# Kernel tuning notes

Hardware: AMD Instinct MI355X
Metric: run time of the kernel (lower is better)

The kernel has to match this reference:

```python
import jax, jax.numpy as jnp
import numpy as np

NEG_INF = jnp.float32(-1e30)  # stand-in for -inf; relu(-inf) == relu(-1e30) == 0


def setup_inputs() -> dict:
    key = jax.random.key(0)
    ks = jax.random.split(key, 8)
    B, S, E = 4, 4096, 512
    query = jax.random.normal(ks[0], (B, S, E), dtype=jnp.float32)
    k_in = jax.random.normal(ks[1], (B, S, E), dtype=jnp.float32)
    v_in = jax.random.normal(ks[2], (B, S, E), dtype=jnp.float32)
    mask = jax.random.randint(ks[3], (B, S, S), 0, 2) > 0  # bool [B,S,S]
    scale = 1.0 / np.sqrt(E)
    W1 = jax.random.uniform(ks[4], (E, E), jnp.float32, -scale, scale)
    b1 = jax.random.uniform(ks[5], (E,), jnp.float32, -scale, scale)
    W2 = jax.random.uniform(ks[6], (E, E), jnp.float32, -scale, scale)
    b2 = jax.random.uniform(ks[7], (E,), jnp.float32, -scale, scale)
    return {"query": query, "key": k_in, "value": v_in, "mask": mask,
            "W1": W1, "b1": b1, "W2": W2, "b2": b2}


def reference(query, key, value, mask, W1, b1, W2, b2):
    # key projection: nn.Linear -> x @ W.T + b
    k = jnp.einsum('bse,fe->bsf', key, W1) + b1
    # raw dot-product correlation scores [B, S, S]
    scores = jnp.einsum('bqe,bke->bqk', query, k)
    # module forces mask[:, :, 0] = True, then fills ~mask with -inf
    m = mask.at[:, :, 0].set(True)
    scores = jnp.where(m, scores, NEG_INF)
    # ReLU instead of softmax (no normalization); dropout is identity in eval
    alpha = jax.nn.relu(scores)
    # value projection then AV matmul
    v = jnp.einsum('bse,fe->bsf', value, W2) + b2
    out = jnp.einsum('bqk,bke->bqe', alpha, v)
    return out
```

## Files before the change

### kernel.cpp

```cpp
#include <hip/hip_runtime.h>
#include <cstdint>


typedef __bf16 bf16x8 __attribute__((ext_vector_type(8)));
typedef float f32x4 __attribute__((ext_vector_type(4)));

__device__ __forceinline__ unsigned short f2bf(float f) {
  unsigned int u = __float_as_uint(f);
  u += 0x7fffu + ((u >> 16) & 1u);
  return (unsigned short)(u >> 16);
}

__device__ __forceinline__ void async_load16(const void* g, void* l) {
  __builtin_amdgcn_global_load_lds(
      (const __attribute__((address_space(1))) unsigned int*)(uintptr_t)g,
      (__attribute__((address_space(3))) unsigned int*)(unsigned int)(uintptr_t)l,
      16, 0, 0);
}

__global__ void __launch_bounds__(256)
prep(const float* __restrict__ q, const float* __restrict__ k,
     const float* __restrict__ v, const float* __restrict__ w1,
     const float* __restrict__ w2, const int* __restrict__ m,
     unsigned short* __restrict__ qb, unsigned short* __restrict__ kb,
     unsigned short* __restrict__ vb, unsigned short* __restrict__ w1b,
     unsigned short* __restrict__ w2b, unsigned int* __restrict__ bits) {
  const int b = blockIdx.x, tid = threadIdx.x;
  if (b < 24576) {
    const int which = b >> 13;
    const int idx = (b & 8191) * 256 + tid;
    const float* in = (which == 0) ? q : (which == 1) ? k : v;
    unsigned short* out = (which == 0) ? qb : (which == 1) ? kb : vb;
    float4 f = ((const float4*)in)[idx];
    ushort4 o;
    o.x = f2bf(f.x); o.y = f2bf(f.y); o.z = f2bf(f.z); o.w = f2bf(f.w);
    ((ushort4*)out)[idx] = o;
  } else if (b < 25088) {
    const int which = (b - 24576) >> 8;
    const int idx = ((b - 24576) & 255) * 256 + tid;
    const float* in = (which == 0) ? w1 : w2;
    unsigned short* out = (which == 0) ? w1b : w2b;
    float4 f = ((const float4*)in)[idx];
    ushort4 o;
    o.x = f2bf(f.x); o.y = f2bf(f.y); o.z = f2bf(f.z); o.w = f2bf(f.w);
    ((ushort4*)out)[idx] = o;
  } else {
    const int lane = tid & 63;
    const size_t wid = (size_t)(b - 25088) * 4 + (tid >> 6);
    const size_t base = wid * 256;
    unsigned long long bl[4];
#pragma unroll
    for (int c = 0; c < 4; ++c) {
      size_t e = base + (size_t)c * 64 + lane;
      int col = (int)(e & 4095);
      bl[c] = __ballot((m[e] != 0) || (col == 0));
    }
    if (lane < 8)
      bits[base / 32 + lane] = (unsigned int)(bl[lane >> 1] >> ((lane & 1) * 32));
  }
}

__global__ void __launch_bounds__(256)
proj(const unsigned short* __restrict__ Kb, const unsigned short* __restrict__ W1b,
     unsigned short* __restrict__ Kp, const float* __restrict__ b1,
     const unsigned short* __restrict__ W2b, const unsigned short* __restrict__ Vb,
     unsigned short* __restrict__ Vpt, const float* __restrict__ b2) {
  constexpr int K = 512;
  constexpr long long SE = 4096LL * 512;
  __shared__ unsigned short sA[2 * 128 * 32];
  __shared__ unsigned short sB[2 * 128 * 32];

  const int L = blockIdx.x;
  const unsigned short *Ab, *Bb;
  unsigned short* C;
  const float* bias;
  int tm0, tn0, N, epi;
  if (L < 512) {
    tn0 = (L & 3) * 128; tm0 = (L >> 2) * 128;
    Ab = Kb; Bb = W1b; C = Kp; bias = b1; N = 512; epi = 0;
  } else {
    const int t = L - 512;
    tn0 = (t & 31) * 128; tm0 = ((t >> 5) & 3) * 128;
    const int bz = t >> 7;
    Ab = W2b; Bb = Vb + (size_t)bz * SE; C = Vpt + (size_t)bz * SE;
    bias = b2; N = 4096; epi = 1;
  }

  const int tid = threadIdx.x;
  const int lane = tid & 63, wave = tid >> 6;
  const int ldrow = lane >> 2, lcol = (lane & 3) * 8;
  const int wm = (wave >> 1) * 64, wn = (wave & 1) * 64;
  const int lr = lane & 15, lq = lane >> 4;

  f32x4 acc[4][4] = {};

  for (int k0 = 0; k0 < K; k0 += 64) {
#pragma unroll
    for (int g = 0; g < 2; ++g)
#pragma unroll
      for (int l = 0; l < 2; ++l) {
        const int row = wave * 32 + l * 16;
        async_load16(Ab + (size_t)(tm0 + row + ldrow) * K + (k0 + g * 32 + lcol),
                     &sA[g * 4096 + row * 32]);
        async_load16(Bb + (size_t)(tn0 + row + ldrow) * K + (k0 + g * 32 + lcol),
                     &sB[g * 4096 + row * 32]);
      }
    __syncthreads();
#pragma unroll
    for (int g = 0; g < 2; ++g) {
      bf16x8 af[4], bfr[4];
#pragma unroll
      for (int t = 0; t < 4; ++t) {
        af[t]  = *(const bf16x8*)&sA[g * 4096 + (wm + t * 16 + lr) * 32 + lq * 8];
        bfr[t] = *(const bf16x8*)&sB[g * 4096 + (wn + t * 16 + lr) * 32 + lq * 8];
      }
#pragma unroll
      for (int mt = 0; mt < 4; ++mt)
#pragma unroll
        for (int nt = 0; nt < 4; ++nt)
          acc[mt][nt] = __builtin_amdgcn_mfma_f32_16x16x32_bf16(af[mt], bfr[nt],
                                                                acc[mt][nt], 0, 0, 0);
    }
    __syncthreads();
  }

#pragma unroll
  for (int mt = 0; mt < 4; ++mt)
#pragma unroll
    for (int r = 0; r < 4; ++r) {
      const int mm = tm0 + wm + mt * 16 + lq * 4 + r;
#pragma unroll
      for (int nt = 0; nt < 4; ++nt) {
        const int n = tn0 + wn + nt * 16 + lr;
        float v = acc[mt][nt][r];
        v += (epi == 0) ? bias[n] : bias[mm];
        C[(size_t)mm * N + n] = f2bf(v);
      }
    }
}

template <int EPI>
__global__ void __launch_bounds__(512, 2)
gemm256(const unsigned short* __restrict__ A, const unsigned short* __restrict__ B,
        void* __restrict__ Cout, const unsigned int* __restrict__ mbits,
        int M, int N, int K,
        long long strA, long long strB, long long strC, long long strM) {
  __shared__ unsigned short sA[2][256][64];
  __shared__ unsigned short sB[2][256][64];

  int lin = blockIdx.x;
  lin = (lin & 7) * ((int)gridDim.x >> 3) + (lin >> 3);
  const int tilesN = N >> 8;
  const int tilesM = M >> 8;
  const int bx = lin % tilesN;
  const int by = (lin / tilesN) % tilesM;
  const int bz = lin / (tilesN * tilesM);

  const int tn0 = bx << 8, tm0 = by << 8;
  const unsigned short* Ab = A + (size_t)bz * strA;
  const unsigned short* Bb = B + (size_t)bz * strB;

  const int tid  = threadIdx.x;
  const int lane = tid & 63;
  const int w    = tid >> 6;
  const int wr   = w >> 2;
  const int wc   = w & 3;
  const int lr   = lane & 15;
  const int lq   = lane >> 4;

  const int srow = tid >> 3;
  const int scol = (((tid & 7) ^ (srow & 7)) << 3);
  const int sdst = tid << 4;

#define STAGE64(bufbase, g, t0, k0, R0)                                      \
  async_load16((g) + (size_t)((t0) + (R0) + srow) * K + (k0) + scol,         \
               (char*)(bufbase) + ((R0) << 7) + sdst)

  const int sxor  = (lr & 7) << 4;
  const int k0off = (lq << 4) ^ sxor;
  const int k1off = (64 | (lq << 4)) ^ sxor;
  const int aRow  = (wr * 128 + lr) * 128;
  const int bRow  = (wc * 64 + lr) * 128;

#define LDA(d, mh, mt2, kk)                                                  \
  (*(const bf16x8*)((const char*)sA[d] + aRow + (mh) * 8192 + (mt2) * 2048 + \
                    k##kk##off))
#define LDB(d, nh, nt2, kk)                                                  \
  (*(const bf16x8*)((const char*)sB[d] + bRow + (nh) * 4096 + (nt2) * 2048 + \
                    k##kk##off))

  f32x4 acc[8][4] = {};
  bf16x8 afr[4][2];
  bf16x8 bfr[4][2];

#define RDA(d, mh)                                                           \
  _Pragma("unroll") for (int mt2 = 0; mt2 < 4; ++mt2) {                      \
    afr[mt2][0] = LDA(d, mh, mt2, 0);                                        \
    afr[mt2][1] = LDA(d, mh, mt2, 1);                                        \
  }
#define RDB(d, nh)                                                           \
  _Pragma("unroll") for (int nt2 = 0; nt2 < 2; ++nt2) {                      \
    bfr[(nh) * 2 + nt2][0] = LDB(d, nh, nt2, 0);                             \
    bfr[(nh) * 2 + nt2][1] = LDB(d, nh, nt2, 1);                             \
  }
#define MFMAQ(mh, nh)                                                        \
  __builtin_amdgcn_s_setprio(1);                                             \
  _Pragma("unroll") for (int mt2 = 0; mt2 < 4; ++mt2)                        \
  _Pragma("unroll") for (int nt2 = 0; nt2 < 2; ++nt2) {                      \
    acc[(mh) * 4 + mt2][(nh) * 2 + nt2] =                                    \
        __builtin_amdgcn_mfma_f32_16x16x32_bf16(                             \
            afr[mt2][0], bfr[(nh) * 2 + nt2][0],                             \
            acc[(mh) * 4 + mt2][(nh) * 2 + nt2], 0, 0, 0);                   \
    acc[(mh) * 4 + mt2][(nh) * 2 + nt2] =                                    \
        __builtin_amdgcn_mfma_f32_16x16x32_bf16(                             \
            afr[mt2][1], bfr[(nh) * 2 + nt2][1],                             \
            acc[(mh) * 4 + mt2][(nh) * 2 + nt2], 0, 0, 0);                   \
  }                                                                          \
  __builtin_amdgcn_s_setprio(0);
#define BAR __builtin_amdgcn_s_barrier()

  const int nIter = K >> 7;

  STAGE64(sB[0], Bb, tn0, 0, 0);   STAGE64(sB[0], Bb, tn0, 0, 64);
  STAGE64(sB[0], Bb, tn0, 0, 128); STAGE64(sB[0], Bb, tn0, 0, 192);
  STAGE64(sA[0], Ab, tm0, 0, 0);   STAGE64(sA[0], Ab, tm0, 0, 64);
  STAGE64(sA[0], Ab, tm0, 0, 128); STAGE64(sA[0], Ab, tm0, 0, 192);
  STAGE64(sB[1], Bb, tn0, 64, 0);  STAGE64(sB[1], Bb, tn0, 64, 64);
  STAGE64(sB[1], Bb, tn0, 64, 128);STAGE64(sB[1], Bb, tn0, 64, 192);
  asm volatile("s_waitcnt vmcnt(4)" ::: "memory");
  BAR;

  for (int j = 0; j < nIter; ++j) {
    const int kb = j << 7;
    const bool pf = (j + 1 < nIter);
    RDA(0, 0); RDB(0, 0);
    STAGE64(sA[1], Ab, tm0, kb + 64, 0);
    STAGE64(sA[1], Ab, tm0, kb + 64, 64);
    BAR; MFMAQ(0, 0); BAR;
    RDB(0, 1);
    STAGE64(sA[1], Ab, tm0, kb + 64, 128);
    STAGE64(sA[1], Ab, tm0, kb + 64, 192);
    BAR; MFMAQ(0, 1); BAR;
    RDA(0, 1);
    if (pf) { STAGE64(sB[0], Bb, tn0, kb + 128, 0);
              STAGE64(sB[0], Bb, tn0, kb + 128, 64); }
    BAR; MFMAQ(1, 1); BAR;
    if (pf) { STAGE64(sB[0], Bb, tn0, kb + 128, 128);
              STAGE64(sB[0], Bb, tn0, kb + 128, 192); }
    BAR; MFMAQ(1, 0);
    if (pf) asm volatile("s_waitcnt vmcnt(4)" ::: "memory");
    else    asm volatile("s_waitcnt vmcnt(0)" ::: "memory");
    BAR;
    RDA(1, 0); RDB(1, 0);
    if (pf) { STAGE64(sA[0], Ab, tm0, kb + 128, 0);
              STAGE64(sA[0], Ab, tm0, kb + 128, 64); }
    BAR; MFMAQ(0, 0); BAR;
    RDB(1, 1);
    if (pf) { STAGE64(sA[0], Ab, tm0, kb + 128, 128);
              STAGE64(sA[0], Ab, tm0, kb + 128, 192); }
    BAR; MFMAQ(0, 1); BAR;
    RDA(1, 1);
    if (pf) { STAGE64(sB[1], Bb, tn0, kb + 192, 0);
              STAGE64(sB[1], Bb, tn0, kb + 192, 64); }
    BAR; MFMAQ(1, 1); BAR;
    if (pf) { STAGE64(sB[1], Bb, tn0, kb + 192, 128);
              STAGE64(sB[1], Bb, tn0, kb + 192, 192); }
    BAR; MFMAQ(1, 0);
    asm volatile("s_waitcnt vmcnt(4)" ::: "memory");
    BAR;
  }

#pragma unroll
  for (int mt = 0; mt < 8; ++mt) {
#pragma unroll
    for (int r = 0; r < 4; ++r) {
      const int m = tm0 + wr * 128 + mt * 16 + lq * 4 + r;
      unsigned long long w64 = 0;
      if constexpr (EPI == 2) {
        w64 = *(const unsigned long long*)&mbits[(size_t)bz * strM +
                                                 (size_t)m * (N >> 5) +
                                                 ((tn0 + wc * 64) >> 5)];
      }
#pragma unroll
      for (int nt = 0; nt < 4; ++nt) {
        const int n = tn0 + wc * 64 + nt * 16 + lr;
        float v = acc[mt][nt][r];
        if constexpr (EPI == 2) {
          v = ((w64 >> (nt * 16 + lr)) & 1ull) ? fmaxf(v, 0.f) : 0.f;
          ((unsigned short*)Cout)[(size_t)bz * strC + (size_t)m * N + n] = f2bf(v);
        } else {
          ((float*)Cout)[(size_t)bz * strC + (size_t)m * N + n] = v;
        }
      }
    }
  }
#undef STAGE64
#undef LDA
#undef LDB
#undef RDA
#undef RDB
#undef MFMAQ
#undef BAR
}

template <int EPI>
__global__ void __launch_bounds__(256)
gemm_bt(const unsigned short* __restrict__ A, const unsigned short* __restrict__ B,
        void* __restrict__ Cout, const unsigned int* __restrict__ mbits,
        int M, int N, int K,
        long long strA, long long strB, long long strC, long long strM) {
  __shared__ unsigned short sA[2 * 128 * 32];
  __shared__ unsigned short sB[2 * 128 * 32];

  const int tid  = threadIdx.x;
  const int lane = tid & 63;
  const int wave = tid >> 6;
  const int bz   = blockIdx.z;
  const int tn0  = blockIdx.x * 128;
  const int tm0  = blockIdx.y * 128;

  const unsigned short* Ab = A + (size_t)bz * strA;
  const unsigned short* Bb = B + (size_t)bz * strB;

  const int ldrow = lane >> 2;
  const int lcol  = (lane & 3) * 8;
  const int wm = (wave >> 1) * 64;
  const int wn = (wave & 1) * 64;
  const int lr = lane & 15;
  const int lq = lane >> 4;

  f32x4 acc[4][4] = {};

  for (int k0 = 0; k0 < K; k0 += 64) {
#pragma unroll
    for (int g = 0; g < 2; ++g)
#pragma unroll
      for (int l = 0; l < 2; ++l) {
        const int row = wave * 32 + l * 16;
        async_load16(Ab + (size_t)(tm0 + row + ldrow) * K + (k0 + g * 32 + lcol),
                     &sA[g * 4096 + row * 32]);
        async_load16(Bb + (size_t)(tn0 + row + ldrow) * K + (k0 + g * 32 + lcol),
                     &sB[g * 4096 + row * 32]);
      }
    __syncthreads();
#pragma unroll
    for (int g = 0; g < 2; ++g) {
      bf16x8 af[4], bfr[4];
#pragma unroll
      for (int t = 0; t < 4; ++t) {
        af[t]  = *(const bf16x8*)&sA[g * 4096 + (wm + t * 16 + lr) * 32 + lq * 8];
        bfr[t] = *(const bf16x8*)&sB[g * 4096 + (wn + t * 16 + lr) * 32 + lq * 8];
      }
#pragma unroll
      for (int mt = 0; mt < 4; ++mt)
#pragma unroll
        for (int nt = 0; nt < 4; ++nt)
          acc[mt][nt] = __builtin_amdgcn_mfma_f32_16x16x32_bf16(af[mt], bfr[nt],
                                                                acc[mt][nt], 0, 0, 0);
    }
    __syncthreads();
  }

#pragma unroll
  for (int mt = 0; mt < 4; ++mt) {
#pragma unroll
    for (int r = 0; r < 4; ++r) {
      const int m = tm0 + wm + mt * 16 + lq * 4 + r;
#pragma unroll
      for (int nt = 0; nt < 4; ++nt) {
        const int n = tn0 + wn + nt * 16 + lr;
        float v = acc[mt][nt][r];
        ((float*)Cout)[(size_t)bz * strC + (size_t)m * N + n] = v;
      }
    }
  }
}

extern "C" void kernel_launch(void* const* d_in, const int* in_sizes, int n_in,
                              void* d_out, int out_size, void* d_ws, size_t ws_size,
                              hipStream_t stream) {
  const float* query = (const float*)d_in[0];
  const float* key   = (const float*)d_in[1];
  const float* value = (const float*)d_in[2];
  const int*   mask  = (const int*)d_in[3];
  const float* W1    = (const float*)d_in[4];
  const float* b1    = (const float*)d_in[5];
  const float* W2    = (const float*)d_in[6];
  const float* b2    = (const float*)d_in[7];
  float* out = (float*)d_out;

  constexpr int B = 4, S = 4096, E = 512;
  constexpr long long BSE = (long long)B * S * E;
  constexpr long long SE  = (long long)S * E;
  constexpr long long SS  = (long long)S * S;
  constexpr long long BSS = (long long)B * S * S;
  constexpr long long EE  = (long long)E * E;

  char* ws = (char*)d_ws;
  unsigned short* Qb   = (unsigned short*)ws;  ws += BSE * 2;
  unsigned short* Kb   = (unsigned short*)ws;  ws += BSE * 2;
  unsigned short* Vb   = (unsigned short*)ws;  ws += BSE * 2;
  unsigned short* W1b  = (unsigned short*)ws;  ws += EE * 2;
  unsigned short* W2b  = (unsigned short*)ws;  ws += EE * 2;
  unsigned short* Kp   = (unsigned short*)ws;  ws += BSE * 2;
  unsigned short* Vpt  = (unsigned short*)ws;  ws += BSE * 2;
  unsigned short* alph = (unsigned short*)ws;  ws += BSS * 2;
  unsigned int*   mbit = (unsigned int*)ws;    ws += BSS / 8;

  prep<<<dim3(24576 + 512 + 65536), 256, 0, stream>>>(
      query, key, value, W1, W2, mask, Qb, Kb, Vb, W1b, W2b, mbit);

  proj<<<dim3(1024), 256, 0, stream>>>(Kb, W1b, Kp, b1, W2b, Vb, Vpt, b2);

  gemm256<2><<<dim3((S / 256) * (S / 256) * B), 512, 0, stream>>>(
      Qb, Kp, alph, mbit, S, S, E, SE, SE, SS, SS / 32);

  gemm_bt<3><<<dim3(E / 128, S / 128, B), 256, 0, stream>>>(
      alph, Vpt, out, nullptr, S, E, S, SS, SE, SE, 0);
}
```

Baseline: 662.6 us.

## Replace AV gemm with pipelined 256x128 tile kernel with swizzled LDS

```diff
diff --git a/kernel.cpp b/kernel.cpp
--- a/kernel.cpp
+++ b/kernel.cpp
@@ -303,77 +303,139 @@
 #undef BAR
 }
 
-template <int EPI>
-__global__ void __launch_bounds__(256)
-gemm_bt(const unsigned short* __restrict__ A, const unsigned short* __restrict__ B,
-        void* __restrict__ Cout, const unsigned int* __restrict__ mbits,
-        int M, int N, int K,
-        long long strA, long long strB, long long strC, long long strM) {
-  __shared__ unsigned short sA[2 * 128 * 32];
-  __shared__ unsigned short sB[2 * 128 * 32];
+__global__ void __launch_bounds__(512, 2)
+outgemm(const unsigned short* __restrict__ A, const unsigned short* __restrict__ B,
+        float* __restrict__ Cout, int M, int N, int K,
+        long long strA, long long strB, long long strC) {
+  __shared__ unsigned short sA[2][256][64];
+  __shared__ unsigned short sB[2][128][64];
+
+  int lin = blockIdx.x;
+  lin = (lin & 7) * ((int)gridDim.x >> 3) + (lin >> 3);
+  const int tilesN = N >> 7;
+  const int tilesM = M >> 8;
+  const int bx = lin % tilesN;
+  const int by = (lin / tilesN) % tilesM;
+  const int bz = lin / (tilesN * tilesM);
+
+  const int tn0 = bx << 7, tm0 = by << 8;
+  const unsigned short* Ab = A + (size_t)bz * strA;
+  const unsigned short* Bb = B + (size_t)bz * strB;
 
   const int tid  = threadIdx.x;
   const int lane = tid & 63;
-  const int wave = tid >> 6;
-  const int bz   = blockIdx.z;
-  const int tn0  = blockIdx.x * 128;
-  const int tm0  = blockIdx.y * 128;
-
-  const unsigned short* Ab = A + (size_t)bz * strA;
-  const unsigned short* Bb = B + (size_t)bz * strB;
-
-  const int ldrow = lane >> 2;
-  const int lcol  = (lane & 3) * 8;
-  const int wm = (wave >> 1) * 64;
-  const int wn = (wave & 1) * 64;
-  const int lr = lane & 15;
-  const int lq = lane >> 4;
-
-  f32x4 acc[4][4] = {};
-
-  for (int k0 = 0; k0 < K; k0 += 64) {
-#pragma unroll
-    for (int g = 0; g < 2; ++g)
-#pragma unroll
-      for (int l = 0; l < 2; ++l) {
-        const int row = wave * 32 + l * 16;
-        async_load16(Ab + (size_t)(tm0 + row + ldrow) * K + (k0 + g * 32 + lcol),
-                     &sA[g * 4096 + row * 32]);
-        async_load16(Bb + (size_t)(tn0 + row + ldrow) * K + (k0 + g * 32 + lcol),
-                     &sB[g * 4096 + row * 32]);
-      }
-    __syncthreads();
-#pragma unroll
-    for (int g = 0; g < 2; ++g) {
-      bf16x8 af[4], bfr[4];
-#pragma unroll
-      for (int t = 0; t < 4; ++t) {
-        af[t]  = *(const bf16x8*)&sA[g * 4096 + (wm + t * 16 + lr) * 32 + lq * 8];
-        bfr[t] = *(const bf16x8*)&sB[g * 4096 + (wn + t * 16 + lr) * 32 + lq * 8];
-      }
-#pragma unroll
-      for (int mt = 0; mt < 4; ++mt)
-#pragma unroll
-        for (int nt = 0; nt < 4; ++nt)
-          acc[mt][nt] = __builtin_amdgcn_mfma_f32_16x16x32_bf16(af[mt], bfr[nt],
-                                                                acc[mt][nt], 0, 0, 0);
+  const int w    = tid >> 6;
+  const int wr   = w >> 2;
+  const int wc   = w & 3;
+  const int lr   = lane & 15;
+  const int lq   = lane >> 4;
+
+  const int srow = tid >> 3;
+  const int scol = (((tid & 7) ^ (srow & 7)) << 3);
+  const int sdst = tid << 4;
+
+#define OST(bufbase, g, t0, k0, R0)                                          \
+  async_load16((g) + (size_t)((t0) + (R0) + srow) * K + (k0) + scol,         \
+               (char*)(bufbase) + ((R0) << 7) + sdst)
+
+  const int sxor  = (lr & 7) << 4;
+  const int k0off = (lq << 4) ^ sxor;
+  const int k1off = (64 | (lq << 4)) ^ sxor;
+  const int aRow  = (wr * 128 + lr) * 128;
+  const int bRow  = (wc * 32 + lr) * 128;
+
+#define OLDA(d, mh, mt2, kk)                                                 \
+  (*(const bf16x8*)((const char*)sA[d] + aRow + (mh) * 8192 + (mt2) * 2048 + \
+                    k##kk##off))
+#define OLDB(d, nt, kk)                                                      \
+  (*(const bf16x8*)((const char*)sB[d] + bRow + (nt) * 2048 + k##kk##off))
+
+  f32x4 acc[8][2] = {};
+  bf16x8 afr[4][2];
+  bf16x8 bfr[2][2];
+
+#define ORDA(d, mh)                                                          \
+  _Pragma("unroll") for (int mt2 = 0; mt2 < 4; ++mt2) {                      \
+    afr[mt2][0] = OLDA(d, mh, mt2, 0);                                       \
+    afr[mt2][1] = OLDA(d, mh, mt2, 1);                                       \
+  }
+#define ORDB(d, nt)                                                          \
+  { bfr[nt][0] = OLDB(d, nt, 0); bfr[nt][1] = OLDB(d, nt, 1); }
+#define OMFMAQ(mh, nt)                                                       \
+  __builtin_amdgcn_s_setprio(1);                                             \
+  _Pragma("unroll") for (int mt2 = 0; mt2 < 4; ++mt2) {                      \
+    acc[(mh) * 4 + mt2][nt] = __builtin_amdgcn_mfma_f32_16x16x32_bf16(       \
+        afr[mt2][0], bfr[nt][0], acc[(mh) * 4 + mt2][nt], 0, 0, 0);          \
+    acc[(mh) * 4 + mt2][nt] = __builtin_amdgcn_mfma_f32_16x16x32_bf16(       \
+        afr[mt2][1], bfr[nt][1], acc[(mh) * 4 + mt2][nt], 0, 0, 0);          \
+  }                                                                          \
+  __builtin_amdgcn_s_setprio(0);
+#define OBAR __builtin_amdgcn_s_barrier()
+
+  const int nIter = K >> 7;
+
+  OST(sB[0], Bb, tn0, 0, 0);   OST(sB[0], Bb, tn0, 0, 64);
+  OST(sA[0], Ab, tm0, 0, 0);   OST(sA[0], Ab, tm0, 0, 64);
+  OST(sA[0], Ab, tm0, 0, 128); OST(sA[0], Ab, tm0, 0, 192);
+  OST(sB[1], Bb, tn0, 64, 0);  OST(sB[1], Bb, tn0, 64, 64);
+  asm volatile("s_waitcnt vmcnt(2)" ::: "memory");
+  OBAR;
+
+  for (int j = 0; j < nIter; ++j) {
+    const int kb = j << 7;
+    const bool pf = (j + 1 < nIter);
+    ORDA(0, 0); ORDB(0, 0);
+    OST(sA[1], Ab, tm0, kb + 64, 0);
+    OST(sA[1], Ab, tm0, kb + 64, 64);
+    OBAR; OMFMAQ(0, 0); OBAR;
+    ORDB(0, 1);
+    OST(sA[1], Ab, tm0, kb + 64, 128);
+    OST(sA[1], Ab, tm0, kb + 64, 192);
+    OBAR; OMFMAQ(0, 1); OBAR;
+    ORDA(0, 1);
+    if (pf) OST(sB[0], Bb, tn0, kb + 128, 0);
+    OBAR; OMFMAQ(1, 1); OBAR;
+    if (pf) OST(sB[0], Bb, tn0, kb + 128, 64);
+    OBAR; OMFMAQ(1, 0);
+    if (pf) asm volatile("s_waitcnt vmcnt(2)" ::: "memory");
+    else    asm volatile("s_waitcnt vmcnt(0)" ::: "memory");
+    OBAR;
+    ORDA(1, 0); ORDB(1, 0);
+    if (pf) { OST(sA[0], Ab, tm0, kb + 128, 0);
+              OST(sA[0], Ab, tm0, kb + 128, 64); }
+    OBAR; OMFMAQ(0, 0); OBAR;
+    ORDB(1, 1);
+    if (pf) { OST(sA[0], Ab, tm0, kb + 128, 128);
+              OST(sA[0], Ab, tm0, kb + 128, 192); }
+    OBAR; OMFMAQ(0, 1); OBAR;
+    ORDA(1, 1);
+    if (pf) OST(sB[1], Bb, tn0, kb + 192, 0);
+    OBAR; OMFMAQ(1, 1); OBAR;
+    if (pf) OST(sB[1], Bb, tn0, kb + 192, 64);
+    OBAR; OMFMAQ(1, 0);
+    asm volatile("s_waitcnt vmcnt(2)" ::: "memory");
+    OBAR;
+  }
+
+#pragma unroll
+  for (int mt = 0; mt < 8; ++mt) {
+#pragma unroll
+    for (int r = 0; r < 4; ++r) {
+      const int m = tm0 + wr * 128 + mt * 16 + lq * 4 + r;
+#pragma unroll
+      for (int nt = 0; nt < 2; ++nt) {
+        const int n = tn0 + wc * 32 + nt * 16 + lr;
+        Cout[(size_t)bz * strC + (size_t)m * N + n] = acc[mt][nt][r];
+      }
     }
-    __syncthreads();
-  }
-
-#pragma unroll
-  for (int mt = 0; mt < 4; ++mt) {
-#pragma unroll
-    for (int r = 0; r < 4; ++r) {
-      const int m = tm0 + wm + mt * 16 + lq * 4 + r;
-#pragma unroll
-      for (int nt = 0; nt < 4; ++nt) {
-        const int n = tn0 + wn + nt * 16 + lr;
-        float v = acc[mt][nt][r];
-        ((float*)Cout)[(size_t)bz * strC + (size_t)m * N + n] = v;
-      }
-    }
-  }
+  }
+#undef OST
+#undef OLDA
+#undef OLDB
+#undef ORDA
+#undef ORDB
+#undef OMFMAQ
+#undef OBAR
 }
 
 extern "C" void kernel_launch(void* const* d_in, const int* in_sizes, int n_in,
@@ -415,6 +477,6 @@
   gemm256<2><<<dim3((S / 256) * (S / 256) * B), 512, 0, stream>>>(
       Qb, Kp, alph, mbit, S, S, E, SE, SE, SS, SS / 32);
 
-  gemm_bt<3><<<dim3(E / 128, S / 128, B), 256, 0, stream>>>(
-      alph, Vpt, out, nullptr, S, E, S, SS, SE, SE, 0);
-}
+  outgemm<<<dim3((E / 128) * (S / 256) * B), 512, 0, stream>>>(
+      alph, Vpt, out, S, E, S, SS, SE, SE);
+}
```

Result: faster. 631.0 us (-4.8%).
